# Kernel optimization log

Hardware: AMD Instinct MI355X
Metric: run time of the kernel (lower is better)

Reference implementation:

```python
import jax, jax.numpy as jnp
import numpy as np

B, T, D, H, O = 1024, 512, 1, 64, 1


def setup_inputs() -> dict:
    key = jax.random.key(0)
    ks = jax.random.split(key, 11)
    s = 1.0 / np.sqrt(H)  # PyTorch LSTM/Linear default uniform init bound

    def u(k, shape):
        return jax.random.uniform(k, shape, jnp.float32, -s, s)

    return {
        "x": jax.random.normal(ks[0], (B, T, D), jnp.float32),
        "W_ih0": u(ks[1], (4 * H, D)),
        "W_hh0": u(ks[2], (4 * H, H)),
        "b_ih0": u(ks[3], (4 * H,)),
        "b_hh0": u(ks[4], (4 * H,)),
        "W_ih1": u(ks[5], (4 * H, H)),
        "W_hh1": u(ks[6], (4 * H, H)),
        "b_ih1": u(ks[7], (4 * H,)),
        "b_hh1": u(ks[8], (4 * H,)),
        "W_fc": u(ks[9], (O, H)),
        "b_fc": u(ks[10], (O,)),
    }


def _lstm_layer(x, W_ih, W_hh, b_ih, b_hh):
    # x: [B, T, Din] -> outputs [B, T, H], final hidden [B, H]
    # Precompute all input projections in one big GEMM (gate order: i, f, g, o)
    xg = jnp.einsum('btd,gd->btg', x, W_ih) + b_ih + b_hh  # [B, T, 4H]
    h0 = jnp.zeros((x.shape[0], W_hh.shape[1]), x.dtype)
    c0 = h0

    def step(carry, xt):
        h, c = carry
        gates = xt + h @ W_hh.T  # [B, 4H]
        i, f, g, o = jnp.split(gates, 4, axis=-1)
        i = jax.nn.sigmoid(i)
        f = jax.nn.sigmoid(f)
        g = jnp.tanh(g)
        o = jax.nn.sigmoid(o)
        c = f * c + i * g
        h = o * jnp.tanh(c)
        return (h, c), h

    (hT, cT), hs = jax.lax.scan(step, (h0, c0), jnp.swapaxes(xg, 0, 1))
    return jnp.swapaxes(hs, 0, 1), hT


def reference(x, W_ih0, W_hh0, b_ih0, b_hh0, W_ih1, W_hh1, b_ih1, b_hh1, W_fc, b_fc):
    y0, h0f = _lstm_layer(x, W_ih0, W_hh0, b_ih0, b_hh0)
    y1, h1f = _lstm_layer(y0, W_ih1, W_hh1, b_ih1, b_hh1)
    # original: h_out.view(-1, H) stacks final hidden of BOTH layers -> [2B, H]
    h_out = jnp.concatenate([h0f, h1f], axis=0)
    return h_out @ W_fc.T + b_fc  # [2B, 1]
```

## Files before the change

### kernel.cpp

```cpp
#include <hip/hip_runtime.h>


typedef _Float16 f16x8 __attribute__((ext_vector_type(8)));
typedef float f32x4 __attribute__((ext_vector_type(4)));

#define TSTEPS 512
#define L2E 1.44269504088896340736f

__device__ __forceinline__ float lstm_point(float ai, float af, float ag, float ao,
                                            float& c) {
    const float p  = __builtin_amdgcn_exp2f(ai);
    const float s_ = __builtin_amdgcn_exp2f(af);
    const float r_ = __builtin_amdgcn_exp2f(ag);
    const float v  = __builtin_amdgcn_exp2f(ao);
    const float m1 = (1.f + p) * (1.f + r_);
    const float R  = __builtin_amdgcn_rcpf(m1 * (1.f + s_));
    const float f  = m1 * R;
    const float ig = (r_ - 1.f) * ((1.f + s_) * R);
    const float cc = __builtin_fmaf(f, c, ig);
    c = cc;
    const float w  = __builtin_amdgcn_exp2f(cc * (2.f * L2E));
    return (w - 1.f) * __builtin_amdgcn_rcpf((1.f + v) * (1.f + w));
}

__global__ __launch_bounds__(512, 2) void lstm2_kernel(
    const float* __restrict__ x,
    const float* __restrict__ W_ih0, const float* __restrict__ W_hh0,
    const float* __restrict__ b_ih0, const float* __restrict__ b_hh0,
    const float* __restrict__ W_ih1, const float* __restrict__ W_hh1,
    const float* __restrict__ b_ih1, const float* __restrict__ b_hh1,
    const float* __restrict__ W_fc,  const float* __restrict__ b_fc,
    float* __restrict__ out)
{
    __shared__ alignas(16) _Float16 H[2][2][256];
    __shared__ alignas(16) float    xl[2][64][4];

    const int tid  = (int)threadIdx.x;
    const int lane = tid & 63;
    const int wid  = tid >> 6;
    const int RL   = wid >> 2;
    const int sw   = wid & 3;
    const int c    = lane & 15;
    const int quad = lane >> 4;
    const int j    = (sw << 4) | c;
    const int b0   = (int)blockIdx.x * 4;

    const int rdOff = quad * 64 + (c & 3) * 16;
    const int wOff  = (j >> 3) * 64 + quad * 16 + (j & 7) * 2;

    float biasc0[4], wih0c[4];
    f32x4 cini1[4];
    f16x8 bfA[4][2];
    f16x8 bfB[4][4];

    if (RL == 0) {
#pragma unroll
        for (int g = 0; g < 4; ++g) {
            const int n = j + 64 * g;
            const float sg = (g == 2) ? (2.0f * L2E) : (-L2E);
            biasc0[g] = sg * (b_ih0[n] + b_hh0[n]);
            wih0c[g]  = sg * W_ih0[n];
#pragma unroll
            for (int kb = 0; kb < 2; ++kb) {
                const float* p = W_hh0 + n * 64 + kb * 32 + quad * 8;
#pragma unroll
                for (int q = 0; q < 8; ++q) bfA[g][kb][q] = (_Float16)(p[q] * sg);
            }
        }
    } else {
#pragma unroll
        for (int g = 0; g < 4; ++g) {
            const int n = j + 64 * g;
            const float sg = (g == 2) ? (2.0f * L2E) : (-L2E);
            const float bb1 = sg * (b_ih1[n] + b_hh1[n]);
            cini1[g][0] = bb1; cini1[g][1] = bb1; cini1[g][2] = bb1; cini1[g][3] = bb1;
#pragma unroll
            for (int kb = 0; kb < 4; ++kb) {
                const int kk = kb * 32 + quad * 8;
                const float* p = (kk < 64) ? (W_ih1 + n * 64 + kk)
                                           : (W_hh1 + n * 64 + (kk - 64));
#pragma unroll
                for (int q = 0; q < 8; ++q) bfB[g][kb][q] = (_Float16)(p[q] * sg);
            }
        }
    }

    for (int i = tid; i < 1024; i += 512) ((_Float16*)H)[i] = (_Float16)0.f;
    if (tid < 256) {
        xl[0][lane][wid] = x[(b0 + wid) * TSTEPS + lane];
    }
    __syncthreads();

    float cst = 0.f;

    if (RL == 0) {
        const float xq = xl[0][0][quad];
        const float hv = lstm_point(__builtin_fmaf(xq, wih0c[0], biasc0[0]),
                                    __builtin_fmaf(xq, wih0c[1], biasc0[1]),
                                    __builtin_fmaf(xq, wih0c[2], biasc0[2]),
                                    __builtin_fmaf(xq, wih0c[3], biasc0[3]), cst);
        *(_Float16*)((char*)H + wOff) = (_Float16)hv;
    }
    __syncthreads();

    char* Hc = (char*)H;
    const char* rdBase = Hc + rdOff;
    char* w0A = Hc + 512  + wOff;
    char* w0B = Hc + 0    + wOff;
    char* w1A = Hc + 1024 + wOff;
    char* w1B = Hc + 1536 + wOff;

    auto SEL = [&](const f32x4& A) -> float {
        const float x01 = (quad & 1) ? A[1] : A[0];
        const float x23 = (quad & 1) ? A[3] : A[2];
        return (quad & 2) ? x23 : x01;
    };

    auto STEP0 = [&](int rimm, char* wp, const f32x4 (&ini)[4]) {
        const f16x8 a0 = *(const f16x8*)(rdBase + rimm);
        const f16x8 a1 = *(const f16x8*)(rdBase + rimm + 256);
        f32x4 A[4];
        __builtin_amdgcn_s_setprio(1);
#pragma unroll
        for (int g = 0; g < 4; ++g) {
            A[g] = __builtin_amdgcn_mfma_f32_16x16x32_f16(a0, bfA[g][0], ini[g], 0, 0, 0);
            A[g] = __builtin_amdgcn_mfma_f32_16x16x32_f16(a1, bfA[g][1], A[g], 0, 0, 0);
        }
        __builtin_amdgcn_s_setprio(0);
        const float hv = lstm_point(SEL(A[0]), SEL(A[1]), SEL(A[2]), SEL(A[3]), cst);
        *(_Float16*)wp = (_Float16)hv;
    };

    auto STEP1 = [&](int r0imm, int r1imm, char* wp) {
        const f16x8 a0 = *(const f16x8*)(rdBase + r0imm);
        const f16x8 a1 = *(const f16x8*)(rdBase + r0imm + 256);
        const f16x8 a2 = *(const f16x8*)(rdBase + r1imm);
        const f16x8 a3 = *(const f16x8*)(rdBase + r1imm + 256);
        f32x4 Bq[4];
        __builtin_amdgcn_s_setprio(1);
#pragma unroll
        for (int g = 0; g < 4; ++g) {
            Bq[g] = __builtin_amdgcn_mfma_f32_16x16x32_f16(a0, bfB[g][0], cini1[g], 0, 0, 0);
            Bq[g] = __builtin_amdgcn_mfma_f32_16x16x32_f16(a1, bfB[g][1], Bq[g], 0, 0, 0);
            Bq[g] = __builtin_amdgcn_mfma_f32_16x16x32_f16(a2, bfB[g][2], Bq[g], 0, 0, 0);
            Bq[g] = __builtin_amdgcn_mfma_f32_16x16x32_f16(a3, bfB[g][3], Bq[g], 0, 0, 0);
        }
        __builtin_amdgcn_s_setprio(0);
        const float hv = lstm_point(SEL(Bq[0]), SEL(Bq[1]), SEL(Bq[2]), SEL(Bq[3]), cst);
        *(_Float16*)wp = (_Float16)hv;
    };

    auto INI = [&](int t, f32x4 (&ini)[4]) {
        const f32x4 xv = *(const f32x4*)&xl[(t >> 6) & 1][t & 63][0];
#pragma unroll
        for (int g = 0; g < 4; ++g) {
            ini[g][0] = __builtin_fmaf(xv[0], wih0c[g], biasc0[g]);
            ini[g][1] = __builtin_fmaf(xv[1], wih0c[g], biasc0[g]);
            ini[g][2] = __builtin_fmaf(xv[2], wih0c[g], biasc0[g]);
            ini[g][3] = __builtin_fmaf(xv[3], wih0c[g], biasc0[g]);
        }
    };

    f32x4 iniN[4], iniB[4];
    if (RL == 0) INI(1, iniN);

    for (int t = 1; t <= 509; t += 2) {
        if (RL == 0) {
            INI(t + 1, iniB);
            STEP0(0, w0A, iniN);
        } else {
            STEP1(0, 1536, w1A);
        }
        __syncthreads();

        const int tB = t + 1;
        if (RL == 0) {
            if ((tB & 63) == 32 && tB < 448) {
                const int cn = (tB >> 6) + 1;
                xl[cn & 1][lane][wid] = x[(b0 + wid) * TSTEPS + cn * 64 + lane];
            }
            INI(t + 2, iniN);
            STEP0(512, w0B, iniB);
        } else {
            STEP1(512, 1024, w1B);
        }
        __syncthreads();
    }

    if (RL == 0) STEP0(0, w0A, iniN);
    else         STEP1(0, 1536, w1A);
    __syncthreads();

    if (RL == 1) STEP1(512, 1024, w1B);
    __syncthreads();

    if (tid < 8) {
        const int which = tid >> 2, b = tid & 3;
        const char* hb = Hc + which * 1024 + 512;
        float s = b_fc[0];
        for (int jj = 0; jj < 64; ++jj) {
            const int off = (jj >> 3) * 64 + b * 16 + (jj & 7) * 2;
            s += (float)*(const _Float16*)(hb + off) * W_fc[jj];
        }
        out[which * 1024 + b0 + b] = s;
    }
}

extern "C" void kernel_launch(void* const* d_in, const int* in_sizes, int n_in,
                              void* d_out, int out_size, void* d_ws, size_t ws_size,
                              hipStream_t stream) {
    (void)in_sizes; (void)n_in; (void)d_ws; (void)ws_size; (void)out_size;
    lstm2_kernel<<<256, 512, 0, stream>>>(
        (const float*)d_in[0],
        (const float*)d_in[1], (const float*)d_in[2],
        (const float*)d_in[3], (const float*)d_in[4],
        (const float*)d_in[5], (const float*)d_in[6],
        (const float*)d_in[7], (const float*)d_in[8],
        (const float*)d_in[9], (const float*)d_in[10],
        (float*)d_out);
}
```

Measured before the change: 285.9 us.

## Split LSTM steps into MFMA and pointwise phases interleaved across layers

Each timestep is split into an MFMA phase and a pointwise tail phase. Layer 0's tail is scheduled to run while layer 1 does its MFMAs, and the reverse, so the two wave groups alternate matrix-core and VALU work. This doubles the number of block barriers per timestep pair, from two to four. The read offset changes so the needed value lands in accumulator element 0, which removes the per-lane select, and bias/x terms are added after the MFMA instead of seeding the accumulator. Launch bounds drop to one block per CU, which gives the compiler more registers but may cost occupancy.

```diff
diff --git a/kernel.cpp b/kernel.cpp
--- a/kernel.cpp
+++ b/kernel.cpp
@@ -23,7 +23,7 @@
     return (w - 1.f) * __builtin_amdgcn_rcpf((1.f + v) * (1.f + w));
 }
 
-__global__ __launch_bounds__(512, 2) void lstm2_kernel(
+__global__ __launch_bounds__(512, 1) void lstm2_kernel(
     const float* __restrict__ x,
     const float* __restrict__ W_ih0, const float* __restrict__ W_hh0,
     const float* __restrict__ b_ih0, const float* __restrict__ b_hh0,
@@ -45,11 +45,10 @@
     const int j    = (sw << 4) | c;
     const int b0   = (int)blockIdx.x * 4;
 
-    const int rdOff = quad * 64 + (c & 3) * 16;
+    const int rdOff = quad * 64 + (c >> 2) * 16;
     const int wOff  = (j >> 3) * 64 + quad * 16 + (j & 7) * 2;
 
-    float biasc0[4], wih0c[4];
-    f32x4 cini1[4];
+    float biasc0[4], wih0c[4], biasc1[4];
     f16x8 bfA[4][2];
     f16x8 bfB[4][4];
 
@@ -72,8 +71,7 @@
         for (int g = 0; g < 4; ++g) {
             const int n = j + 64 * g;
             const float sg = (g == 2) ? (2.0f * L2E) : (-L2E);
-            const float bb1 = sg * (b_ih1[n] + b_hh1[n]);
-            cini1[g][0] = bb1; cini1[g][1] = bb1; cini1[g][2] = bb1; cini1[g][3] = bb1;
+            biasc1[g] = sg * (b_ih1[n] + b_hh1[n]);
 #pragma unroll
             for (int kb = 0; kb < 4; ++kb) {
                 const int kk = kb * 32 + quad * 8;
@@ -86,12 +84,65 @@
     }
 
     for (int i = tid; i < 1024; i += 512) ((_Float16*)H)[i] = (_Float16)0.f;
-    if (tid < 256) {
-        xl[0][lane][wid] = x[(b0 + wid) * TSTEPS + lane];
-    }
+    if (tid < 256) xl[0][lane][wid] = x[(b0 + wid) * TSTEPS + lane];
     __syncthreads();
 
     float cst = 0.f;
+    char* Hc = (char*)H;
+    const char* rdBase = Hc + rdOff;
+    char* wp0a = Hc + 512  + wOff;
+    char* wp0b = Hc + 0    + wOff;
+    char* wp1a = Hc + 1024 + wOff;
+    char* wp1b = Hc + 1536 + wOff;
+
+    const f32x4 zf4 = {0.f, 0.f, 0.f, 0.f};
+    f32x4 acc0[4], acc1[4];
+    f16x8 pa0, pa1;
+    float preA[4], preB[4];
+
+    auto MFMA0 = [&](int rimm) {
+        const f16x8 a0 = *(const f16x8*)(rdBase + rimm);
+        const f16x8 a1 = *(const f16x8*)(rdBase + rimm + 256);
+        __builtin_amdgcn_s_setprio(1);
+#pragma unroll
+        for (int g = 0; g < 4; ++g) {
+            acc0[g] = __builtin_amdgcn_mfma_f32_16x16x32_f16(a0, bfA[g][0], zf4, 0, 0, 0);
+            acc0[g] = __builtin_amdgcn_mfma_f32_16x16x32_f16(a1, bfA[g][1], acc0[g], 0, 0, 0);
+        }
+        __builtin_amdgcn_s_setprio(0);
+    };
+    auto TAIL0 = [&](char* wp, const float (&pre)[4]) {
+        const float hv = lstm_point(acc0[0][0] + pre[0], acc0[1][0] + pre[1],
+                                    acc0[2][0] + pre[2], acc0[3][0] + pre[3], cst);
+        *(_Float16*)wp = (_Float16)hv;
+    };
+    auto PRE0 = [&](int t, float (&pre)[4]) {
+        const float xq = xl[(t >> 6) & 1][t & 63][quad];
+#pragma unroll
+        for (int g = 0; g < 4; ++g) pre[g] = __builtin_fmaf(xq, wih0c[g], biasc0[g]);
+    };
+    auto PREF1 = [&](int rimm) {
+        pa0 = *(const f16x8*)(rdBase + rimm);
+        pa1 = *(const f16x8*)(rdBase + rimm + 256);
+    };
+    auto MFMA1 = [&](int r1imm) {
+        const f16x8 a2 = *(const f16x8*)(rdBase + r1imm);
+        const f16x8 a3 = *(const f16x8*)(rdBase + r1imm + 256);
+        __builtin_amdgcn_s_setprio(1);
+#pragma unroll
+        for (int g = 0; g < 4; ++g) {
+            acc1[g] = __builtin_amdgcn_mfma_f32_16x16x32_f16(pa0, bfB[g][0], zf4, 0, 0, 0);
+            acc1[g] = __builtin_amdgcn_mfma_f32_16x16x32_f16(pa1, bfB[g][1], acc1[g], 0, 0, 0);
+            acc1[g] = __builtin_amdgcn_mfma_f32_16x16x32_f16(a2,  bfB[g][2], acc1[g], 0, 0, 0);
+            acc1[g] = __builtin_amdgcn_mfma_f32_16x16x32_f16(a3,  bfB[g][3], acc1[g], 0, 0, 0);
+        }
+        __builtin_amdgcn_s_setprio(0);
+    };
+    auto TAIL1 = [&](char* wp) {
+        const float hv = lstm_point(acc1[0][0] + biasc1[0], acc1[1][0] + biasc1[1],
+                                    acc1[2][0] + biasc1[2], acc1[3][0] + biasc1[3], cst);
+        *(_Float16*)wp = (_Float16)hv;
+    };
 
     if (RL == 0) {
         const float xq = xl[0][0][quad];
@@ -99,99 +150,57 @@
                                     __builtin_fmaf(xq, wih0c[1], biasc0[1]),
                                     __builtin_fmaf(xq, wih0c[2], biasc0[2]),
                                     __builtin_fmaf(xq, wih0c[3], biasc0[3]), cst);
-        *(_Float16*)((char*)H + wOff) = (_Float16)hv;
-    }
-    __syncthreads();
-
-    char* Hc = (char*)H;
-    const char* rdBase = Hc + rdOff;
-    char* w0A = Hc + 512  + wOff;
-    char* w0B = Hc + 0    + wOff;
-    char* w1A = Hc + 1024 + wOff;
-    char* w1B = Hc + 1536 + wOff;
-
-    auto SEL = [&](const f32x4& A) -> float {
-        const float x01 = (quad & 1) ? A[1] : A[0];
-        const float x23 = (quad & 1) ? A[3] : A[2];
-        return (quad & 2) ? x23 : x01;
-    };
-
-    auto STEP0 = [&](int rimm, char* wp, const f32x4 (&ini)[4]) {
-        const f16x8 a0 = *(const f16x8*)(rdBase + rimm);
-        const f16x8 a1 = *(const f16x8*)(rdBase + rimm + 256);
-        f32x4 A[4];
-        __builtin_amdgcn_s_setprio(1);
-#pragma unroll
-        for (int g = 0; g < 4; ++g) {
-            A[g] = __builtin_amdgcn_mfma_f32_16x16x32_f16(a0, bfA[g][0], ini[g], 0, 0, 0);
-            A[g] = __builtin_amdgcn_mfma_f32_16x16x32_f16(a1, bfA[g][1], A[g], 0, 0, 0);
-        }
-        __builtin_amdgcn_s_setprio(0);
-        const float hv = lstm_point(SEL(A[0]), SEL(A[1]), SEL(A[2]), SEL(A[3]), cst);
-        *(_Float16*)wp = (_Float16)hv;
-    };
-
-    auto STEP1 = [&](int r0imm, int r1imm, char* wp) {
-        const f16x8 a0 = *(const f16x8*)(rdBase + r0imm);
-        const f16x8 a1 = *(const f16x8*)(rdBase + r0imm + 256);
-        const f16x8 a2 = *(const f16x8*)(rdBase + r1imm);
-        const f16x8 a3 = *(const f16x8*)(rdBase + r1imm + 256);
-        f32x4 Bq[4];
-        __builtin_amdgcn_s_setprio(1);
-#pragma unroll
-        for (int g = 0; g < 4; ++g) {
-            Bq[g] = __builtin_amdgcn_mfma_f32_16x16x32_f16(a0, bfB[g][0], cini1[g], 0, 0, 0);
-            Bq[g] = __builtin_amdgcn_mfma_f32_16x16x32_f16(a1, bfB[g][1], Bq[g], 0, 0, 0);
-            Bq[g] = __builtin_amdgcn_mfma_f32_16x16x32_f16(a2, bfB[g][2], Bq[g], 0, 0, 0);
-            Bq[g] = __builtin_amdgcn_mfma_f32_16x16x32_f16(a3, bfB[g][3], Bq[g], 0, 0, 0);
-        }
-        __builtin_amdgcn_s_setprio(0);
-        const float hv = lstm_point(SEL(Bq[0]), SEL(Bq[1]), SEL(Bq[2]), SEL(Bq[3]), cst);
-        *(_Float16*)wp = (_Float16)hv;
-    };
-
-    auto INI = [&](int t, f32x4 (&ini)[4]) {
-        const f32x4 xv = *(const f32x4*)&xl[(t >> 6) & 1][t & 63][0];
-#pragma unroll
-        for (int g = 0; g < 4; ++g) {
-            ini[g][0] = __builtin_fmaf(xv[0], wih0c[g], biasc0[g]);
-            ini[g][1] = __builtin_fmaf(xv[1], wih0c[g], biasc0[g]);
-            ini[g][2] = __builtin_fmaf(xv[2], wih0c[g], biasc0[g]);
-            ini[g][3] = __builtin_fmaf(xv[3], wih0c[g], biasc0[g]);
-        }
-    };
-
-    f32x4 iniN[4], iniB[4];
-    if (RL == 0) INI(1, iniN);
+        *(_Float16*)(Hc + wOff) = (_Float16)hv;
+        PRE0(1, preA);
+    }
+    __syncthreads();
+
+    if (RL == 0) MFMA0(0); else PREF1(0);
+    __syncthreads();
 
     for (int t = 1; t <= 509; t += 2) {
         if (RL == 0) {
-            INI(t + 1, iniB);
-            STEP0(0, w0A, iniN);
-        } else {
-            STEP1(0, 1536, w1A);
-        }
-        __syncthreads();
-
-        const int tB = t + 1;
-        if (RL == 0) {
-            if ((tB & 63) == 32 && tB < 448) {
-                const int cn = (tB >> 6) + 1;
+            TAIL0(wp0a, preA);
+            PRE0(t + 1, preB);
+            if ((t & 63) == 31 && t < 448) {
+                const int cn = (t >> 6) + 1;
                 xl[cn & 1][lane][wid] = x[(b0 + wid) * TSTEPS + cn * 64 + lane];
             }
-            INI(t + 2, iniN);
-            STEP0(512, w0B, iniB);
-        } else {
-            STEP1(512, 1024, w1B);
-        }
-        __syncthreads();
-    }
-
-    if (RL == 0) STEP0(0, w0A, iniN);
-    else         STEP1(0, 1536, w1A);
-    __syncthreads();
-
-    if (RL == 1) STEP1(512, 1024, w1B);
+        } else {
+            MFMA1(1536);
+        }
+        __syncthreads();
+        if (RL == 0) {
+            MFMA0(512);
+        } else {
+            TAIL1(wp1a);
+            PREF1(512);
+        }
+        __syncthreads();
+        if (RL == 0) {
+            TAIL0(wp0b, preB);
+            PRE0(t + 2, preA);
+        } else {
+            MFMA1(1024);
+        }
+        __syncthreads();
+        if (RL == 0) {
+            MFMA0(0);
+        } else {
+            TAIL1(wp1b);
+            PREF1(0);
+        }
+        __syncthreads();
+    }
+
+    if (RL == 0) TAIL0(wp0a, preA);
+    else         MFMA1(1536);
+    __syncthreads();
+    if (RL == 1) { TAIL1(wp1a); PREF1(512); }
+    __syncthreads();
+    if (RL == 1) MFMA1(1024);
+    __syncthreads();
+    if (RL == 1) TAIL1(wp1b);
     __syncthreads();
 
     if (tid < 8) {
```

Result: slower. 328.5 us (+14.9%).
